# Kernel tuning notes

Hardware: AMD Instinct MI355X
Metric: run time of the kernel (lower is better)

The kernel has to match this reference:

```python
import jax, jax.numpy as jnp
import numpy as np

INPUT_DIM = 1024
HIDDEN_DIM = 1024
NUM_HEADS = 16
HEAD_DIM = HIDDEN_DIM // NUM_HEADS


def setup_inputs() -> dict:
    key = jax.random.key(0)
    ks = jax.random.split(key, 11)
    B, S = 2, 2048
    s_in = 1.0 / np.sqrt(INPUT_DIM)
    s_hid = 1.0 / np.sqrt(HIDDEN_DIM)
    return {
        "query": jax.random.normal(ks[0], (B, S, INPUT_DIM), jnp.float32),
        "key": jax.random.normal(ks[1], (B, S, INPUT_DIM), jnp.float32),
        "value": jax.random.normal(ks[2], (B, S, INPUT_DIM), jnp.float32),
        "Wq": jax.random.normal(ks[3], (INPUT_DIM, HIDDEN_DIM), jnp.float32) * s_in,
        "bq": jnp.zeros((HIDDEN_DIM,), jnp.float32),
        "Wk": jax.random.normal(ks[4], (INPUT_DIM, HEAD_DIM), jnp.float32) * s_in,
        "bk": jnp.zeros((HEAD_DIM,), jnp.float32),
        "Wv": jax.random.normal(ks[5], (INPUT_DIM, HEAD_DIM), jnp.float32) * s_in,
        "bv": jnp.zeros((HEAD_DIM,), jnp.float32),
        "Wo": jax.random.normal(ks[6], (HIDDEN_DIM, INPUT_DIM), jnp.float32) * s_hid,
        "bo": jnp.zeros((INPUT_DIM,), jnp.float32),
    }


def reference(query, key, value, Wq, bq, Wk, bk, Wv, bv, Wo, bo):
    B, S, _ = query.shape
    # projections
    q = query @ Wq + bq                       # [B,S,H*D]
    k = key @ Wk + bk                         # [B,S,D]  (single shared head)
    v = value @ Wv + bv                       # [B,S,D]
    q = q.reshape(B, S, NUM_HEADS, HEAD_DIM)  # [B,S,H,D]
    # MQA scores: shared K broadcast over query heads
    scores = jnp.einsum('bqhd,bkd->bhqk', q, k) / np.sqrt(HIDDEN_DIM)
    attn = jax.nn.softmax(scores, axis=-1)    # [B,H,Q,K]
    out = jnp.einsum('bhqk,bkd->bqhd', attn, v)  # [B,Q,H,D]
    out = out.reshape(B, S, HIDDEN_DIM)
    return out @ Wo + bo
```

## Files before the change

### kernel.cpp

```cpp
#include <hip/hip_runtime.h>


typedef unsigned int   u32;
typedef unsigned short u16;
typedef union { float4 v; float f[4]; } f4u;
typedef __attribute__((ext_vector_type(8)))  short frag16;
typedef __attribute__((ext_vector_type(4)))  float f32x4;
typedef __attribute__((ext_vector_type(16))) float f32x16;
typedef union { frag16 v; u32 w[4]; u16 e[8]; } bf8u;

static __device__ __forceinline__ u16 f2bf(float x) {
  union { float f; u32 u; } v; v.f = x;
  u32 r = v.u + 0x7fff + ((v.u >> 16) & 1);
  return (u16)(r >> 16);
}

static __device__ __forceinline__ u32 cvt_pk_bf16(float lo, float hi) {
  u32 r;
  asm("v_cvt_pk_bf16_f32 %0, %1, %2" : "=v"(r) : "v"(lo), "v"(hi));
  return r;
}

static __device__ __forceinline__ void pl32_swap(u32& a, u32& b) {
  asm volatile("v_permlane32_swap_b32 %0, %1" : "+v"(a), "+v"(b));
}

static __device__ __forceinline__ void gload_lds16(const u16* g, u16* l) {
  __builtin_amdgcn_global_load_lds(
      (const __attribute__((address_space(1))) u32*)g,
      (__attribute__((address_space(3))) u32*)l, 16, 0, 0);
}

static __device__ void tcvt_tile(const float* __restrict__ src,
                                 u16* __restrict__ dst,
                                 int C, int ldT, int rt, int ct,
                                 float (*t)[65]) {
  const int r0 = rt * 64, c0 = ct * 64;
  const int tr  = threadIdx.x >> 4;
  const int tc4 = (threadIdx.x & 15) * 4;
#pragma unroll
  for (int i = 0; i < 4; ++i) {
    f4u v; v.v = *(const float4*)(src + (size_t)(r0 + tr + i * 16) * C + c0 + tc4);
    t[tr + i * 16][tc4 + 0] = v.f[0];
    t[tr + i * 16][tc4 + 1] = v.f[1];
    t[tr + i * 16][tc4 + 2] = v.f[2];
    t[tr + i * 16][tc4 + 3] = v.f[3];
  }
  __syncthreads();
#pragma unroll
  for (int i = 0; i < 4; ++i) {
    const int oc = tr + i * 16;
    ushort4 o;
    o.x = f2bf(t[tc4 + 0][oc]);
    o.y = f2bf(t[tc4 + 1][oc]);
    o.z = f2bf(t[tc4 + 2][oc]);
    o.w = f2bf(t[tc4 + 3][oc]);
    *(ushort4*)(dst + (size_t)(c0 + oc) * ldT + r0 + tc4) = o;
  }
}

__global__ __launch_bounds__(256)
void prep_w(const float* __restrict__ Wq, const float* __restrict__ Wo,
            const float* __restrict__ Wk, const float* __restrict__ Wv,
            const float* __restrict__ query,
            u16* __restrict__ wq_t, u16* __restrict__ wo_t,
            u16* __restrict__ wk_t, u16* __restrict__ wv_t,
            u16* __restrict__ xq_bf) {
  const int bid = blockIdx.x;
  if (bid >= 544) {
    const size_t base = (size_t)(bid - 544) * 4096 + threadIdx.x * 16;
    f4u x0, x1, x2, x3;
    x0.v = *(const float4*)(query + base);
    x1.v = *(const float4*)(query + base + 4);
    x2.v = *(const float4*)(query + base + 8);
    x3.v = *(const float4*)(query + base + 12);
    bf8u t0, t1;
    t0.w[0] = cvt_pk_bf16(x0.f[0], x0.f[1]);
    t0.w[1] = cvt_pk_bf16(x0.f[2], x0.f[3]);
    t0.w[2] = cvt_pk_bf16(x1.f[0], x1.f[1]);
    t0.w[3] = cvt_pk_bf16(x1.f[2], x1.f[3]);
    t1.w[0] = cvt_pk_bf16(x2.f[0], x2.f[1]);
    t1.w[1] = cvt_pk_bf16(x2.f[2], x2.f[3]);
    t1.w[2] = cvt_pk_bf16(x3.f[0], x3.f[1]);
    t1.w[3] = cvt_pk_bf16(x3.f[2], x3.f[3]);
    *(frag16*)(xq_bf + base)     = t0.v;
    *(frag16*)(xq_bf + base + 8) = t1.v;
    return;
  }
  __shared__ float t[64][65];
  if (bid < 256)      tcvt_tile(Wq, wq_t, 1024, 1024, bid >> 4, bid & 15, t);
  else if (bid < 512) tcvt_tile(Wo, wo_t, 1024, 1024, (bid - 256) >> 4, (bid - 256) & 15, t);
  else if (bid < 528) tcvt_tile(Wk, wk_t, 64, 1024, bid - 512, 0, t);
  else                tcvt_tile(Wv, wv_t, 64, 1024, bid - 528, 0, t);
}

static __device__ void gemm128n64(const u16* __restrict__ Abf,
                                  const u16* __restrict__ Bt,
                                  const float* __restrict__ bias,
                                  void* __restrict__ Cout, int out_mode,
                                  float oscale, int row0, int col0,
                                  int N, int K, u16* As, u16* Bs) {
  const int tid  = threadIdx.x;
  const int lane = tid & 63;
  const int quad = lane >> 4, l15 = lane & 15;
  const int w = tid >> 6, wy = w >> 1, wx = w & 1;
  const int lrow = lane >> 3, lcol = (lane & 7) * 8;

  f32x4 acc[4][2];
#pragma unroll
  for (int i = 0; i < 4; ++i)
#pragma unroll
    for (int j = 0; j < 2; ++j) {
      acc[i][j][0] = 0.f; acc[i][j][1] = 0.f;
      acc[i][j][2] = 0.f; acc[i][j][3] = 0.f;
    }

  const u16* ag = Abf + (size_t)(row0 + w * 32 + lrow) * K + lcol;
  const u16* bg = Bt  + (size_t)(col0 + w * 16 + lrow) * K + lcol;
  u16* alds = As + w * 4 * 512;
  u16* blds = Bs + w * 2 * 512;

#pragma unroll
  for (int i = 0; i < 4; ++i)
    gload_lds16(ag + (size_t)i * 8 * K, alds + i * 512);
#pragma unroll
  for (int i = 0; i < 2; ++i)
    gload_lds16(bg + (size_t)i * 8 * K, blds + i * 512);
  __syncthreads();

  for (int k0 = 0; k0 < K; k0 += 64) {
    frag16 af[2][4], bfr[2][2];
#pragma unroll
    for (int ks = 0; ks < 2; ++ks) {
#pragma unroll
      for (int i = 0; i < 4; ++i)
        af[ks][i] = *(const frag16*)(&As[(wy * 64 + i * 16 + l15) * 64 + ks * 32 + quad * 8]);
#pragma unroll
      for (int j = 0; j < 2; ++j)
        bfr[ks][j] = *(const frag16*)(&Bs[(wx * 32 + j * 16 + l15) * 64 + ks * 32 + quad * 8]);
    }
    __syncthreads();

    if (k0 + 64 < K) {
#pragma unroll
      for (int i = 0; i < 4; ++i)
        gload_lds16(ag + (size_t)i * 8 * K + k0 + 64, alds + i * 512);
#pragma unroll
      for (int i = 0; i < 2; ++i)
        gload_lds16(bg + (size_t)i * 8 * K + k0 + 64, blds + i * 512);
    }

#pragma unroll
    for (int ks = 0; ks < 2; ++ks)
#pragma unroll
      for (int i = 0; i < 4; ++i)
#pragma unroll
        for (int j = 0; j < 2; ++j)
          acc[i][j] = __builtin_amdgcn_mfma_f32_16x16x32_bf16(af[ks][i], bfr[ks][j], acc[i][j], 0, 0, 0);

    __syncthreads();
  }

  float bj[2];
#pragma unroll
  for (int j = 0; j < 2; ++j)
    bj[j] = bias[col0 + wx * 32 + j * 16 + l15];

#pragma unroll
  for (int i = 0; i < 4; ++i)
#pragma unroll
    for (int rr = 0; rr < 4; ++rr) {
      const size_t row = row0 + wy * 64 + i * 16 + quad * 4 + rr;
#pragma unroll
      for (int j = 0; j < 2; ++j) {
        const float v = (acc[i][j][rr] + bj[j]) * oscale;
        const int col = col0 + wx * 32 + j * 16 + l15;
        if (out_mode == 0) ((float*)Cout)[row * N + col] = v;
        else               ((u16*)Cout)[row * N + col] = f2bf(v);
      }
    }
}

#define GP 72
template <bool A_FP32>
static __device__ void gemm64(const float* __restrict__ Af32,
                              const u16* __restrict__ Abf,
                              const u16* __restrict__ Bt,
                              const float* __restrict__ bias,
                              void* __restrict__ Cout, int out_mode,
                              float oscale,
                              int row0, int col0, int N, int K, int ldT,
                              u16* As, u16* Bs) {
  const int tid  = threadIdx.x;
  const int lane = tid & 63;
  const int quad = lane >> 4, l15 = lane & 15;
  const int w = tid >> 6, wy = w >> 1, wx = w & 1;

  f32x4 acc[2][2];
#pragma unroll
  for (int i = 0; i < 2; ++i)
#pragma unroll
    for (int j = 0; j < 2; ++j) {
      acc[i][j][0] = 0.f; acc[i][j][1] = 0.f;
      acc[i][j][2] = 0.f; acc[i][j][3] = 0.f;
    }

  const int r = tid >> 2, c16 = (tid & 3) * 16;

  for (int k0 = 0; k0 < K; k0 += 64) {
    frag16 a0, a1;
    if (A_FP32) {
      const float* ap = Af32 + (size_t)(row0 + r) * K + k0 + c16;
      f4u x0, x1, x2, x3;
      x0.v = *(const float4*)(ap);
      x1.v = *(const float4*)(ap + 4);
      x2.v = *(const float4*)(ap + 8);
      x3.v = *(const float4*)(ap + 12);
      bf8u t0, t1;
      t0.w[0] = cvt_pk_bf16(x0.f[0], x0.f[1]);
      t0.w[1] = cvt_pk_bf16(x0.f[2], x0.f[3]);
      t0.w[2] = cvt_pk_bf16(x1.f[0], x1.f[1]);
      t0.w[3] = cvt_pk_bf16(x1.f[2], x1.f[3]);
      t1.w[0] = cvt_pk_bf16(x2.f[0], x2.f[1]);
      t1.w[1] = cvt_pk_bf16(x2.f[2], x2.f[3]);
      t1.w[2] = cvt_pk_bf16(x3.f[0], x3.f[1]);
      t1.w[3] = cvt_pk_bf16(x3.f[2], x3.f[3]);
      a0 = t0.v; a1 = t1.v;
    } else {
      const u16* ap = Abf + (size_t)(row0 + r) * K + k0 + c16;
      a0 = *(const frag16*)(ap);
      a1 = *(const frag16*)(ap + 8);
    }
    const u16* bp = Bt + (size_t)(col0 + r) * K + k0 + c16;
    const frag16 b0 = *(const frag16*)(bp);
    const frag16 b1 = *(const frag16*)(bp + 8);
    __syncthreads();
    *(frag16*)(&As[r * GP + c16])     = a0;
    *(frag16*)(&As[r * GP + c16 + 8]) = a1;
    *(frag16*)(&Bs[r * GP + c16])     = b0;
    *(frag16*)(&Bs[r * GP + c16 + 8]) = b1;
    __syncthreads();
#pragma unroll
    for (int ks = 0; ks < 2; ++ks) {
      frag16 af[2], bf[2];
#pragma unroll
      for (int i = 0; i < 2; ++i)
        af[i] = *(const frag16*)(&As[(wy * 32 + i * 16 + l15) * GP + ks * 32 + quad * 8]);
#pragma unroll
      for (int j = 0; j < 2; ++j)
        bf[j] = *(const frag16*)(&Bs[(wx * 32 + j * 16 + l15) * GP + ks * 32 + quad * 8]);
#pragma unroll
      for (int i = 0; i < 2; ++i)
#pragma unroll
        for (int j = 0; j < 2; ++j)
          acc[i][j] = __builtin_amdgcn_mfma_f32_16x16x32_bf16(af[i], bf[j], acc[i][j], 0, 0, 0);
    }
  }

  float bj[2];
#pragma unroll
  for (int j = 0; j < 2; ++j)
    bj[j] = bias[col0 + wx * 32 + j * 16 + l15];

#pragma unroll
  for (int i = 0; i < 2; ++i) {
#pragma unroll
    for (int rr = 0; rr < 4; ++rr) {
      const size_t row = row0 + wy * 32 + i * 16 + quad * 4 + rr;
#pragma unroll
      for (int j = 0; j < 2; ++j) {
        const float v = (acc[i][j][rr] + bj[j]) * oscale;
        const int col = col0 + wx * 32 + j * 16 + l15;
        if (out_mode == 0)      ((float*)Cout)[row * N + col] = v;
        else if (out_mode == 1) ((u16*)Cout)[row * N + col] = f2bf(v);
        else                    ((u16*)Cout)[(size_t)col * ldT + row] = f2bf(v);
      }
    }
  }
}

#define C2_SCALE 0.045084220027780106f

__global__ __launch_bounds__(256, 4)
void proj2(const float* __restrict__ key, const float* __restrict__ value,
           const u16* __restrict__ xq_bf,
           const u16* __restrict__ wq_t, const u16* __restrict__ wk_t,
           const u16* __restrict__ wv_t,
           const float* __restrict__ bq, const float* __restrict__ bk,
           const float* __restrict__ bv,
           u16* __restrict__ q_bf, u16* __restrict__ k_bf,
           u16* __restrict__ vt_bf, int M, int K) {
  __shared__ __align__(16) u16 smem[12288];
  const int bid = blockIdx.x;
  if (bid < 512)
    gemm128n64(xq_bf, wq_t, bq, q_bf, 1, C2_SCALE,
               (bid >> 4) * 128, (bid & 15) * 64, 1024, K, smem, smem + 8192);
  else if (bid < 576)
    gemm64<true>(key, nullptr, wk_t, bk, k_bf, 1, 1.0f,
                 (bid - 512) * 64, 0, 64, K, 0, smem, smem + 64 * GP);
  else
    gemm64<true>(value, nullptr, wv_t, bv, vt_bf, 2, 1.0f,
                 (bid - 576) * 64, 0, 64, K, M, smem, smem + 64 * GP);
}

__global__ __launch_bounds__(256, 4)
void out_proj(const u16* __restrict__ ao, const u16* __restrict__ wo_t,
              const float* __restrict__ bo, float* __restrict__ out,
              int M, int K) {
  __shared__ __align__(16) u16 smem[12288];
  const int bid = blockIdx.x;
  gemm128n64(ao, wo_t, bo, out, 0, 1.0f,
             (bid >> 4) * 128, (bid & 15) * 64, 1024, K, smem, smem + 8192);
}

#define PP 72

__global__ __launch_bounds__(512, 1)
void mqa_flash_mfma(const u16* __restrict__ Qb,
                    const u16* __restrict__ Kb,
                    const u16* __restrict__ Vt,
                    u16* __restrict__ O) {
  const int S = 2048, HID = 1024, D = 64, BS = 4096;
  __shared__ __align__(16) u16 Kss[64 * PP];
  __shared__ __align__(16) u16 Vss[64 * PP];
  __shared__ float lred[8][32];

  const int tid  = threadIdx.x;
  const int lane = tid & 63;
  const int w    = tid >> 6;
  const int l31  = lane & 31;
  const int hh   = lane >> 5;
  const int qb = blockIdx.x, hg = blockIdx.y, b = blockIdx.z;
  const int h = hg * 8 + w;

  const int sr = tid >> 3;
  const int sc = (tid & 7) * 8;

  const u16* kfb0 = &Kss[l31 * PP + hh * 8];
  const u16* kfb1 = &Kss[(32 + l31) * PP + hh * 8];
  const u16* vfb0 = &Vss[l31 * PP + hh * 8];
  const u16* vfb1 = &Vss[(32 + l31) * PP + hh * 8];
  u16* kw = &Kss[sr * PP + sc];
  u16* vw = &Vss[sr * PP + sc];

  const u16* qrow = Qb + (size_t)(b * S + qb * 32 + l31) * HID + h * D;
  frag16 qf[4];
#pragma unroll
  for (int ks = 0; ks < 4; ++ks)
    qf[ks] = *(const frag16*)(qrow + ks * 16 + hh * 8);

  f32x16 zero16;
#pragma unroll
  for (int r = 0; r < 16; ++r) zero16[r] = 0.f;
  f32x16 oa0, oa1;
#pragma unroll
  for (int r = 0; r < 16; ++r) { oa0[r] = 0.f; oa1[r] = 0.f; }
  float l_lane = 0.f;

  const u16* kbase = Kb + (size_t)(b * S) * D;
  const u16* vbase = Vt + (size_t)(b * S);

  frag16 pk = *(const frag16*)(kbase + (size_t)sr * D + sc);
  frag16 pv = *(const frag16*)(vbase + (size_t)sr * BS + sc);
  *(frag16*)kw = pk;
  *(frag16*)vw = pv;
  pk = *(const frag16*)(kbase + (size_t)(64 + sr) * D + sc);
  pv = *(const frag16*)(vbase + (size_t)sr * BS + 64 + sc);
  __syncthreads();

  for (int kc = 0; kc < S; kc += 64) {
    frag16 kf0[4], kf1[4], vf0[4], vf1[4];
#pragma unroll
    for (int ks = 0; ks < 4; ++ks) {
      kf0[ks] = *(const frag16*)(kfb0 + ks * 16);
      kf1[ks] = *(const frag16*)(kfb1 + ks * 16);
      vf0[ks] = *(const frag16*)(vfb0 + ks * 16);
      vf1[ks] = *(const frag16*)(vfb1 + ks * 16);
    }
    __syncthreads();

    *(frag16*)kw = pk;
    *(frag16*)vw = pv;

    const int nc = (kc + 128 < S) ? kc + 128 : (S - 64);
    pk = *(const frag16*)(kbase + (size_t)(nc + sr) * D + sc);
    pv = *(const frag16*)(vbase + (size_t)sr * BS + nc + sc);

    f32x16 sa0, sa1;
#pragma unroll
    for (int ks = 0; ks < 4; ++ks)
      sa0 = __builtin_amdgcn_mfma_f32_32x32x16_bf16(kf0[ks], qf[ks], ks ? sa0 : zero16, 0, 0, 0);
#pragma unroll
    for (int ks = 0; ks < 4; ++ks)
      sa1 = __builtin_amdgcn_mfma_f32_32x32x16_bf16(kf1[ks], qf[ks], ks ? sa1 : zero16, 0, 0, 0);

    u32 c0[4], c1[4], d0[4], d1[4];
#pragma unroll
    for (int g = 0; g < 4; ++g) {
      const float p0 = __builtin_amdgcn_exp2f(sa0[g * 4 + 0]);
      const float p1 = __builtin_amdgcn_exp2f(sa0[g * 4 + 1]);
      const float p2 = __builtin_amdgcn_exp2f(sa0[g * 4 + 2]);
      const float p3 = __builtin_amdgcn_exp2f(sa0[g * 4 + 3]);
      const float q0 = __builtin_amdgcn_exp2f(sa1[g * 4 + 0]);
      const float q1 = __builtin_amdgcn_exp2f(sa1[g * 4 + 1]);
      const float q2 = __builtin_amdgcn_exp2f(sa1[g * 4 + 2]);
      const float q3 = __builtin_amdgcn_exp2f(sa1[g * 4 + 3]);
      l_lane += ((p0 + p1) + (p2 + p3)) + ((q0 + q1) + (q2 + q3));
      c0[g] = cvt_pk_bf16(p0, p1); c1[g] = cvt_pk_bf16(p2, p3);
      d0[g] = cvt_pk_bf16(q0, q1); d1[g] = cvt_pk_bf16(q2, q3);
    }

    bf8u pa[4];
    pl32_swap(c0[0], c0[1]); pa[0].w[0] = c0[0]; pa[0].w[2] = c0[1];
    pl32_swap(c1[0], c1[1]); pa[0].w[1] = c1[0]; pa[0].w[3] = c1[1];
    pl32_swap(c0[2], c0[3]); pa[1].w[0] = c0[2]; pa[1].w[2] = c0[3];
    pl32_swap(c1[2], c1[3]); pa[1].w[1] = c1[2]; pa[1].w[3] = c1[3];
    pl32_swap(d0[0], d0[1]); pa[2].w[0] = d0[0]; pa[2].w[2] = d0[1];
    pl32_swap(d1[0], d1[1]); pa[2].w[1] = d1[0]; pa[2].w[3] = d1[1];
    pl32_swap(d0[2], d0[3]); pa[3].w[0] = d0[2]; pa[3].w[2] = d0[3];
    pl32_swap(d1[2], d1[3]); pa[3].w[1] = d1[2]; pa[3].w[3] = d1[3];

#pragma unroll
    for (int ks = 0; ks < 4; ++ks) {
      oa0 = __builtin_amdgcn_mfma_f32_32x32x16_bf16(pa[ks].v, vf0[ks], oa0, 0, 0, 0);
      oa1 = __builtin_amdgcn_mfma_f32_32x32x16_bf16(pa[ks].v, vf1[ks], oa1, 0, 0, 0);
    }

    __syncthreads();
  }

  l_lane += __shfl_xor(l_lane, 32);
  lred[w][l31] = l_lane;

#pragma unroll
  for (int g2 = 0; g2 < 4; ++g2) {
    const f32x4 lv = *(const f32x4*)(&lred[w][g2 * 8 + hh * 4]);
#pragma unroll
    for (int m = 0; m < 4; ++m) {
      const int r = g2 * 4 + m;
      const int q_local = g2 * 8 + hh * 4 + m;
      const float li = 1.f / lv[m];
      u16* orow = O + (size_t)(b * S + qb * 32 + q_local) * HID + h * D;
      orow[l31]      = f2bf(oa0[r] * li);
      orow[32 + l31] = f2bf(oa1[r] * li);
    }
  }
}

extern "C" void kernel_launch(void* const* d_in, const int* in_sizes, int n_in,
                              void* d_out, int out_size, void* d_ws, size_t ws_size,
                              hipStream_t stream) {
  const float* query = (const float*)d_in[0];
  const float* key   = (const float*)d_in[1];
  const float* value = (const float*)d_in[2];
  const float* Wq    = (const float*)d_in[3];
  const float* bq    = (const float*)d_in[4];
  const float* Wk    = (const float*)d_in[5];
  const float* bk    = (const float*)d_in[6];
  const float* Wv    = (const float*)d_in[7];
  const float* bv    = (const float*)d_in[8];
  const float* Wo    = (const float*)d_in[9];
  const float* bo    = (const float*)d_in[10];
  float* out = (float*)d_out;

  const int B = 2, S = 2048, IN = 1024, HID = 1024, H = 16, D = 64;
  const int M = B * S;
  const size_t MB = 1024 * 1024;

  char* ws = (char*)d_ws;
  u16* q_bf  = (u16*)ws;
  u16* ao_bf = (u16*)(ws + 8 * MB);
  u16* xq_bf = ao_bf;
  u16* k_bf  = (u16*)(ws + 16 * MB);
  u16* vt_bf = (u16*)(ws + 16 * MB + 512 * 1024);
  u16* wq_t  = (u16*)(ws + 17 * MB);
  u16* wo_t  = (u16*)(ws + 19 * MB);
  u16* wk_t  = (u16*)(ws + 21 * MB);
  u16* wv_t  = (u16*)(ws + 21 * MB + 128 * 1024);

  dim3 blk(256);
  prep_w<<<dim3(1568), blk, 0, stream>>>(Wq, Wo, Wk, Wv, query,
                                         wq_t, wo_t, wk_t, wv_t, xq_bf);
  proj2<<<dim3(640), blk, 0, stream>>>(key, value, xq_bf, wq_t, wk_t, wv_t,
                                       bq, bk, bv, q_bf, k_bf, vt_bf, M, IN);
  mqa_flash_mfma<<<dim3(S / 32, H / 8, B), dim3(512), 0, stream>>>(q_bf, k_bf, vt_bf, ao_bf);
  out_proj<<<dim3(512), blk, 0, stream>>>(ao_bf, wo_t, bo, out, M, HID);
}
```

Measured before the change: 197.2 us.

## Move Wo transpose-convert from prep kernel into extra attention blocks

Removes the Wo transpose/bf16 conversion tiles from the prep kernel and runs them on an extra z-slice of the attention grid, where each 512-thread block converts two 64x64 tiles using shared memory unioned with the attention buffers. The aim is to shorten the prep kernel on the critical path ahead of the projections and to overlap the Wo conversion with attention work. The extra blocks could add tail work to the attention launch, and the shared-memory union may raise LDS usage per block.

```diff
diff --git a/kernel.cpp b/kernel.cpp
--- a/kernel.cpp
+++ b/kernel.cpp
@@ -34,10 +34,10 @@
 static __device__ void tcvt_tile(const float* __restrict__ src,
                                  u16* __restrict__ dst,
                                  int C, int ldT, int rt, int ct,
-                                 float (*t)[65]) {
+                                 float (*t)[65], int tid) {
   const int r0 = rt * 64, c0 = ct * 64;
-  const int tr  = threadIdx.x >> 4;
-  const int tc4 = (threadIdx.x & 15) * 4;
+  const int tr  = tid >> 4;
+  const int tc4 = (tid & 15) * 4;
 #pragma unroll
   for (int i = 0; i < 4; ++i) {
     f4u v; v.v = *(const float4*)(src + (size_t)(r0 + tr + i * 16) * C + c0 + tc4);
@@ -60,15 +60,13 @@
 }
 
 __global__ __launch_bounds__(256)
-void prep_w(const float* __restrict__ Wq, const float* __restrict__ Wo,
-            const float* __restrict__ Wk, const float* __restrict__ Wv,
-            const float* __restrict__ query,
-            u16* __restrict__ wq_t, u16* __restrict__ wo_t,
-            u16* __restrict__ wk_t, u16* __restrict__ wv_t,
-            u16* __restrict__ xq_bf) {
+void prep_w(const float* __restrict__ Wq, const float* __restrict__ Wk,
+            const float* __restrict__ Wv, const float* __restrict__ query,
+            u16* __restrict__ wq_t, u16* __restrict__ wk_t,
+            u16* __restrict__ wv_t, u16* __restrict__ xq_bf) {
   const int bid = blockIdx.x;
-  if (bid >= 544) {
-    const size_t base = (size_t)(bid - 544) * 4096 + threadIdx.x * 16;
+  if (bid >= 288) {
+    const size_t base = (size_t)(bid - 288) * 4096 + threadIdx.x * 16;
     f4u x0, x1, x2, x3;
     x0.v = *(const float4*)(query + base);
     x1.v = *(const float4*)(query + base + 4);
@@ -88,10 +86,9 @@
     return;
   }
   __shared__ float t[64][65];
-  if (bid < 256)      tcvt_tile(Wq, wq_t, 1024, 1024, bid >> 4, bid & 15, t);
-  else if (bid < 512) tcvt_tile(Wo, wo_t, 1024, 1024, (bid - 256) >> 4, (bid - 256) & 15, t);
-  else if (bid < 528) tcvt_tile(Wk, wk_t, 64, 1024, bid - 512, 0, t);
-  else                tcvt_tile(Wv, wv_t, 64, 1024, bid - 528, 0, t);
+  if (bid < 256)      tcvt_tile(Wq, wq_t, 1024, 1024, bid >> 4, bid & 15, t, threadIdx.x);
+  else if (bid < 272) tcvt_tile(Wk, wk_t, 64, 1024, bid - 256, 0, t, threadIdx.x);
+  else                tcvt_tile(Wv, wv_t, 64, 1024, bid - 272, 0, t, threadIdx.x);
 }
 
 static __device__ void gemm128n64(const u16* __restrict__ Abf,
@@ -319,11 +316,26 @@
 void mqa_flash_mfma(const u16* __restrict__ Qb,
                     const u16* __restrict__ Kb,
                     const u16* __restrict__ Vt,
-                    u16* __restrict__ O) {
+                    u16* __restrict__ O,
+                    const float* __restrict__ Wo,
+                    u16* __restrict__ wo_t) {
   const int S = 2048, HID = 1024, D = 64, BS = 4096;
-  __shared__ __align__(16) u16 Kss[64 * PP];
-  __shared__ __align__(16) u16 Vss[64 * PP];
-  __shared__ float lred[8][32];
+  __shared__ __align__(16) union {
+    struct { u16 Kss[64 * PP]; u16 Vss[64 * PP]; float lred[8][32]; } m;
+    float t[2][64][65];
+  } sm;
+
+  if (blockIdx.z == 2) {
+    const int half = threadIdx.x >> 8;
+    const int ltid = threadIdx.x & 255;
+    const int tile = ((blockIdx.y * 64 + blockIdx.x) << 1) | half;
+    tcvt_tile(Wo, wo_t, 1024, 1024, tile >> 4, tile & 15, sm.t[half], ltid);
+    return;
+  }
+
+  u16* Kss = sm.m.Kss;
+  u16* Vss = sm.m.Vss;
+  float (*lred)[32] = sm.m.lred;
 
   const int tid  = threadIdx.x;
   const int lane = tid & 63;
@@ -479,10 +491,11 @@
   u16* wv_t  = (u16*)(ws + 21 * MB + 128 * 1024);
 
   dim3 blk(256);
-  prep_w<<<dim3(1568), blk, 0, stream>>>(Wq, Wo, Wk, Wv, query,
-                                         wq_t, wo_t, wk_t, wv_t, xq_bf);
+  prep_w<<<dim3(1312), blk, 0, stream>>>(Wq, Wk, Wv, query,
+                                         wq_t, wk_t, wv_t, xq_bf);
   proj2<<<dim3(640), blk, 0, stream>>>(key, value, xq_bf, wq_t, wk_t, wv_t,
                                        bq, bk, bv, q_bf, k_bf, vt_bf, M, IN);
-  mqa_flash_mfma<<<dim3(S / 32, H / 8, B), dim3(512), 0, stream>>>(q_bf, k_bf, vt_bf, ao_bf);
+  mqa_flash_mfma<<<dim3(S / 32, H / 8, B + 1), dim3(512), 0, stream>>>(
+      q_bf, k_bf, vt_bf, ao_bf, Wo, wo_t);
   out_proj<<<dim3(512), blk, 0, stream>>>(ao_bf, wo_t, bo, out, M, HID);
 }
```

Result: no change. 197.8 us (+0.3%).

## Double-buffer K/V shared tiles in MQA flash kernel to drop a barrier

Applied to the files above, without the earlier changes.

Splits the K/V shared-memory staging into A/B ping-pong buffers and unrolls the key loop by two. Each half reads from one buffer while writing the prefetched next tile into the other, so only one __syncthreads per 64-key chunk is needed instead of two. This cuts barrier stalls, at the cost of doubling the K/V LDS footprint and adding some code size and register pressure from the unroll.

```diff
diff --git a/kernel.cpp b/kernel.cpp
--- a/kernel.cpp
+++ b/kernel.cpp
@@ -321,8 +321,10 @@
                     const u16* __restrict__ Vt,
                     u16* __restrict__ O) {
   const int S = 2048, HID = 1024, D = 64, BS = 4096;
-  __shared__ __align__(16) u16 Kss[64 * PP];
-  __shared__ __align__(16) u16 Vss[64 * PP];
+  __shared__ __align__(16) u16 KssA[64 * PP];
+  __shared__ __align__(16) u16 VssA[64 * PP];
+  __shared__ __align__(16) u16 KssB[64 * PP];
+  __shared__ __align__(16) u16 VssB[64 * PP];
   __shared__ float lred[8][32];
 
   const int tid  = threadIdx.x;
@@ -336,12 +338,18 @@
   const int sr = tid >> 3;
   const int sc = (tid & 7) * 8;
 
-  const u16* kfb0 = &Kss[l31 * PP + hh * 8];
-  const u16* kfb1 = &Kss[(32 + l31) * PP + hh * 8];
-  const u16* vfb0 = &Vss[l31 * PP + hh * 8];
-  const u16* vfb1 = &Vss[(32 + l31) * PP + hh * 8];
-  u16* kw = &Kss[sr * PP + sc];
-  u16* vw = &Vss[sr * PP + sc];
+  const u16* kfA0 = &KssA[l31 * PP + hh * 8];
+  const u16* kfA1 = &KssA[(32 + l31) * PP + hh * 8];
+  const u16* vfA0 = &VssA[l31 * PP + hh * 8];
+  const u16* vfA1 = &VssA[(32 + l31) * PP + hh * 8];
+  const u16* kfB0 = &KssB[l31 * PP + hh * 8];
+  const u16* kfB1 = &KssB[(32 + l31) * PP + hh * 8];
+  const u16* vfB0 = &VssB[l31 * PP + hh * 8];
+  const u16* vfB1 = &VssB[(32 + l31) * PP + hh * 8];
+  u16* kwA = &KssA[sr * PP + sc];
+  u16* vwA = &VssA[sr * PP + sc];
+  u16* kwB = &KssB[sr * PP + sc];
+  u16* vwB = &VssB[sr * PP + sc];
 
   const u16* qrow = Qb + (size_t)(b * S + qb * 32 + l31) * HID + h * D;
   frag16 qf[4];
@@ -360,74 +368,79 @@
   const u16* kbase = Kb + (size_t)(b * S) * D;
   const u16* vbase = Vt + (size_t)(b * S);
 
-  frag16 pk = *(const frag16*)(kbase + (size_t)sr * D + sc);
-  frag16 pv = *(const frag16*)(vbase + (size_t)sr * BS + sc);
-  *(frag16*)kw = pk;
-  *(frag16*)vw = pv;
+  frag16 pk, pv;
+
+  pk = *(const frag16*)(kbase + (size_t)sr * D + sc);
+  pv = *(const frag16*)(vbase + (size_t)sr * BS + sc);
+  *(frag16*)kwA = pk;
+  *(frag16*)vwA = pv;
   pk = *(const frag16*)(kbase + (size_t)(64 + sr) * D + sc);
   pv = *(const frag16*)(vbase + (size_t)sr * BS + 64 + sc);
   __syncthreads();
 
-  for (int kc = 0; kc < S; kc += 64) {
-    frag16 kf0[4], kf1[4], vf0[4], vf1[4];
-#pragma unroll
-    for (int ks = 0; ks < 4; ++ks) {
-      kf0[ks] = *(const frag16*)(kfb0 + ks * 16);
-      kf1[ks] = *(const frag16*)(kfb1 + ks * 16);
-      vf0[ks] = *(const frag16*)(vfb0 + ks * 16);
-      vf1[ks] = *(const frag16*)(vfb1 + ks * 16);
-    }
-    __syncthreads();
-
-    *(frag16*)kw = pk;
-    *(frag16*)vw = pv;
-
-    const int nc = (kc + 128 < S) ? kc + 128 : (S - 64);
-    pk = *(const frag16*)(kbase + (size_t)(nc + sr) * D + sc);
-    pv = *(const frag16*)(vbase + (size_t)sr * BS + nc + sc);
-
-    f32x16 sa0, sa1;
-#pragma unroll
-    for (int ks = 0; ks < 4; ++ks)
-      sa0 = __builtin_amdgcn_mfma_f32_32x32x16_bf16(kf0[ks], qf[ks], ks ? sa0 : zero16, 0, 0, 0);
-#pragma unroll
-    for (int ks = 0; ks < 4; ++ks)
-      sa1 = __builtin_amdgcn_mfma_f32_32x32x16_bf16(kf1[ks], qf[ks], ks ? sa1 : zero16, 0, 0, 0);
-
-    u32 c0[4], c1[4], d0[4], d1[4];
-#pragma unroll
-    for (int g = 0; g < 4; ++g) {
-      const float p0 = __builtin_amdgcn_exp2f(sa0[g * 4 + 0]);
-      const float p1 = __builtin_amdgcn_exp2f(sa0[g * 4 + 1]);
-      const float p2 = __builtin_amdgcn_exp2f(sa0[g * 4 + 2]);
-      const float p3 = __builtin_amdgcn_exp2f(sa0[g * 4 + 3]);
-      const float q0 = __builtin_amdgcn_exp2f(sa1[g * 4 + 0]);
-      const float q1 = __builtin_amdgcn_exp2f(sa1[g * 4 + 1]);
-      const float q2 = __builtin_amdgcn_exp2f(sa1[g * 4 + 2]);
-      const float q3 = __builtin_amdgcn_exp2f(sa1[g * 4 + 3]);
-      l_lane += ((p0 + p1) + (p2 + p3)) + ((q0 + q1) + (q2 + q3));
-      c0[g] = cvt_pk_bf16(p0, p1); c1[g] = cvt_pk_bf16(p2, p3);
-      d0[g] = cvt_pk_bf16(q0, q1); d1[g] = cvt_pk_bf16(q2, q3);
-    }
-
-    bf8u pa[4];
-    pl32_swap(c0[0], c0[1]); pa[0].w[0] = c0[0]; pa[0].w[2] = c0[1];
-    pl32_swap(c1[0], c1[1]); pa[0].w[1] = c1[0]; pa[0].w[3] = c1[1];
-    pl32_swap(c0[2], c0[3]); pa[1].w[0] = c0[2]; pa[1].w[2] = c0[3];
-    pl32_swap(c1[2], c1[3]); pa[1].w[1] = c1[2]; pa[1].w[3] = c1[3];
-    pl32_swap(d0[0], d0[1]); pa[2].w[0] = d0[0]; pa[2].w[2] = d0[1];
-    pl32_swap(d1[0], d1[1]); pa[2].w[1] = d1[0]; pa[2].w[3] = d1[1];
-    pl32_swap(d0[2], d0[3]); pa[3].w[0] = d0[2]; pa[3].w[2] = d0[3];
-    pl32_swap(d1[2], d1[3]); pa[3].w[1] = d1[2]; pa[3].w[3] = d1[3];
-
-#pragma unroll
-    for (int ks = 0; ks < 4; ++ks) {
-      oa0 = __builtin_amdgcn_mfma_f32_32x32x16_bf16(pa[ks].v, vf0[ks], oa0, 0, 0, 0);
-      oa1 = __builtin_amdgcn_mfma_f32_32x32x16_bf16(pa[ks].v, vf1[ks], oa1, 0, 0, 0);
-    }
-
-    __syncthreads();
-  }
+#define MQA_HALF(KF0, KF1, VF0, VF1, KWN, VWN, CHUNK)                          \
+  {                                                                            \
+    frag16 kf0[4], kf1[4], vf0[4], vf1[4];                                     \
+    _Pragma("unroll")                                                          \
+    for (int ks = 0; ks < 4; ++ks) {                                           \
+      kf0[ks] = *(const frag16*)(KF0 + ks * 16);                               \
+      kf1[ks] = *(const frag16*)(KF1 + ks * 16);                               \
+      vf0[ks] = *(const frag16*)(VF0 + ks * 16);                               \
+      vf1[ks] = *(const frag16*)(VF1 + ks * 16);                               \
+    }                                                                          \
+    *(frag16*)KWN = pk;                                                        \
+    *(frag16*)VWN = pv;                                                        \
+    const int nc_ = ((CHUNK) + 128 < S) ? (CHUNK) + 128 : (S - 64);            \
+    pk = *(const frag16*)(kbase + (size_t)(nc_ + sr) * D + sc);                \
+    pv = *(const frag16*)(vbase + (size_t)sr * BS + nc_ + sc);                 \
+    f32x16 sa0, sa1;                                                           \
+    _Pragma("unroll")                                                          \
+    for (int ks = 0; ks < 4; ++ks)                                             \
+      sa0 = __builtin_amdgcn_mfma_f32_32x32x16_bf16(kf0[ks], qf[ks],           \
+                ks ? sa0 : zero16, 0, 0, 0);                                   \
+    _Pragma("unroll")                                                          \
+    for (int ks = 0; ks < 4; ++ks)                                             \
+      sa1 = __builtin_amdgcn_mfma_f32_32x32x16_bf16(kf1[ks], qf[ks],           \
+                ks ? sa1 : zero16, 0, 0, 0);                                   \
+    u32 c0[4], c1[4], d0[4], d1[4];                                            \
+    _Pragma("unroll")                                                          \
+    for (int g = 0; g < 4; ++g) {                                              \
+      const float p0 = __builtin_amdgcn_exp2f(sa0[g * 4 + 0]);                 \
+      const float p1 = __builtin_amdgcn_exp2f(sa0[g * 4 + 1]);                 \
+      const float p2 = __builtin_amdgcn_exp2f(sa0[g * 4 + 2]);                 \
+      const float p3 = __builtin_amdgcn_exp2f(sa0[g * 4 + 3]);                 \
+      const float q0 = __builtin_amdgcn_exp2f(sa1[g * 4 + 0]);                 \
+      const float q1 = __builtin_amdgcn_exp2f(sa1[g * 4 + 1]);                 \
+      const float q2 = __builtin_amdgcn_exp2f(sa1[g * 4 + 2]);                 \
+      const float q3 = __builtin_amdgcn_exp2f(sa1[g * 4 + 3]);                 \
+      l_lane += ((p0 + p1) + (p2 + p3)) + ((q0 + q1) + (q2 + q3));             \
+      c0[g] = cvt_pk_bf16(p0, p1); c1[g] = cvt_pk_bf16(p2, p3);                \
+      d0[g] = cvt_pk_bf16(q0, q1); d1[g] = cvt_pk_bf16(q2, q3);                \
+    }                                                                          \
+    bf8u pa[4];                                                                \
+    pl32_swap(c0[0], c0[1]); pa[0].w[0] = c0[0]; pa[0].w[2] = c0[1];           \
+    pl32_swap(c1[0], c1[1]); pa[0].w[1] = c1[0]; pa[0].w[3] = c1[1];           \
+    pl32_swap(c0[2], c0[3]); pa[1].w[0] = c0[2]; pa[1].w[2] = c0[3];           \
+    pl32_swap(c1[2], c1[3]); pa[1].w[1] = c1[2]; pa[1].w[3] = c1[3];           \
+    pl32_swap(d0[0], d0[1]); pa[2].w[0] = d0[0]; pa[2].w[2] = d0[1];           \
+    pl32_swap(d1[0], d1[1]); pa[2].w[1] = d1[0]; pa[2].w[3] = d1[1];           \
+    pl32_swap(d0[2], d0[3]); pa[3].w[0] = d0[2]; pa[3].w[2] = d0[3];           \
+    pl32_swap(d1[2], d1[3]); pa[3].w[1] = d1[2]; pa[3].w[3] = d1[3];           \
+    _Pragma("unroll")                                                          \
+    for (int ks = 0; ks < 4; ++ks) {                                           \
+      oa0 = __builtin_amdgcn_mfma_f32_32x32x16_bf16(pa[ks].v, vf0[ks], oa0,    \
+                                                    0, 0, 0);                  \
+      oa1 = __builtin_amdgcn_mfma_f32_32x32x16_bf16(pa[ks].v, vf1[ks], oa1,    \
+                                                    0, 0, 0);                  \
+    }                                                                          \
+    __syncthreads();                                                           \
+  }
+
+  for (int kc = 0; kc < S; kc += 128) {
+    MQA_HALF(kfA0, kfA1, vfA0, vfA1, kwB, vwB, kc);
+    MQA_HALF(kfB0, kfB1, vfB0, vfB1, kwA, vwA, kc + 64);
+  }
+#undef MQA_HALF
 
   l_lane += __shfl_xor(l_lane, 32);
   lred[w][l31] = l_lane;
```

New measurement: 195.4 us. Within noise of the previous version (-0.9%).
